# Kernel tuning notes

Hardware: AMD Instinct MI355X
Metric: run time of the kernel (lower is better)

The kernel has to match this reference:

```python
import jax, jax.numpy as jnp
import numpy as np

NUM_HEADS = 16
NUM_KV_HEADS = 2
HEAD_DIM = 256
HIDDEN = 2048
ROT_DIM = 64          # head_dim * partial_rotary_factor (0.25)
ROPE_THETA = 10000.0
EPS = 1e-6
T = 4096


def setup_inputs() -> dict:
    key = jax.random.key(0)
    k1, k2, k3, k4, k5 = jax.random.split(key, 5)
    qkv_out = HEAD_DIM * (NUM_HEADS * 2 + 2 * NUM_KV_HEADS)  # 9216 (q+gate, k, v)
    return {
        "hidden_states": jax.random.normal(k1, (T, HIDDEN), dtype=jnp.float32),
        "positions": jnp.arange(T, dtype=jnp.int32),
        "w_qkv": jax.random.normal(k2, (HIDDEN, qkv_out), dtype=jnp.float32) * 0.02,
        "w_o": jax.random.normal(k3, (NUM_HEADS * HEAD_DIM, HIDDEN), dtype=jnp.float32) * 0.02,
        "q_norm_w": jax.random.normal(k4, (HEAD_DIM,), dtype=jnp.float32) * 0.1,
        "k_norm_w": jax.random.normal(k5, (HEAD_DIM,), dtype=jnp.float32) * 0.1,
    }


def _gemma_rmsnorm(x, w):
    # GemmaRMSNorm: fp32 compute, scale by (1 + weight)
    xf = x.astype(jnp.float32)
    xf = xf * jax.lax.rsqrt(jnp.mean(xf * xf, axis=-1, keepdims=True) + EPS)
    return (xf * (1.0 + w.astype(jnp.float32))).astype(x.dtype)


def _apply_rope(x, positions):
    # neox-style partial RoPE on first ROT_DIM dims; x: [T, H, D]
    half = ROT_DIM // 2
    inv_freq = 1.0 / (ROPE_THETA ** (jnp.arange(0, ROT_DIM, 2, dtype=jnp.float32) / ROT_DIM))
    freqs = positions.astype(jnp.float32)[:, None] * inv_freq  # [T, half]
    cos = jnp.cos(freqs)[:, None, :]  # [T, 1, half]
    sin = jnp.sin(freqs)[:, None, :]
    x1 = x[..., :half]
    x2 = x[..., half:ROT_DIM]
    rot = jnp.concatenate([x1 * cos - x2 * sin, x2 * cos + x1 * sin], axis=-1)
    return jnp.concatenate([rot, x[..., ROT_DIM:]], axis=-1)


def reference(hidden_states, positions, w_qkv, w_o, q_norm_w, k_norm_w):
    q_size = NUM_HEADS * HEAD_DIM
    kv_size = NUM_KV_HEADS * HEAD_DIM
    qkv = hidden_states @ w_qkv  # [T, 2*q_size + 2*kv_size]

    # split q+gate (interleaved per head), k, v
    q_gate = qkv[:, : 2 * q_size].reshape(-1, NUM_HEADS, 2 * HEAD_DIM)
    q = q_gate[..., :HEAD_DIM]          # [T, H, D]
    gate = q_gate[..., HEAD_DIM:]       # [T, H, D]
    k = qkv[:, 2 * q_size : 2 * q_size + kv_size].reshape(-1, NUM_KV_HEADS, HEAD_DIM)
    v = qkv[:, 2 * q_size + kv_size :].reshape(-1, NUM_KV_HEADS, HEAD_DIM)

    # per-head QK RMSNorm then partial RoPE
    q = _apply_rope(_gemma_rmsnorm(q, q_norm_w), positions)
    k = _apply_rope(_gemma_rmsnorm(k, k_norm_w), positions)

    # GQA causal attention
    rep = NUM_HEADS // NUM_KV_HEADS
    k_rep = jnp.repeat(k, rep, axis=1)  # [T, H, D]
    v_rep = jnp.repeat(v, rep, axis=1)
    scaling = HEAD_DIM ** -0.5
    scores = jnp.einsum("qhd,khd->hqk", q, k_rep) * scaling  # [H, T, T]
    causal = positions[:, None] >= positions[None, :]
    scores = jnp.where(causal[None, :, :], scores, jnp.finfo(scores.dtype).min)
    probs = jax.nn.softmax(scores, axis=-1)
    attn = jnp.einsum("hqk,khd->qhd", probs, v_rep)  # [T, H, D]

    # sigmoid-gated output, then O projection
    attn = attn * jax.nn.sigmoid(gate)
    return attn.reshape(-1, NUM_HEADS * HEAD_DIM) @ w_o
```

## Files before the change

### kernel.cpp

```cpp
#include <hip/hip_runtime.h>

typedef __attribute__((ext_vector_type(4))) float f32x4;
typedef __attribute__((ext_vector_type(8))) __bf16 bf16x8;
typedef unsigned short ushort_t;
typedef unsigned int uint_t;
typedef __attribute__((ext_vector_type(4))) uint_t u32x4;

__device__ __forceinline__ float bf2f(ushort_t u) {
  union { uint_t i; float f; } v; v.i = ((uint_t)u) << 16; return v.f;
}
__device__ __forceinline__ ushort_t f2bf(float f) {
  union { float f; uint_t i; } v; v.f = f;
  uint_t x = v.i;
  return (ushort_t)((x + 0x7fffu + ((x >> 16) & 1u)) >> 16);
}

__device__ __forceinline__ void gload_lds16(const void* g, void* l) {
  __builtin_amdgcn_global_load_lds(
      (const __attribute__((address_space(1))) void*)g,
      (__attribute__((address_space(3))) void*)l, 16, 0, 0);
}

__global__ __launch_bounds__(256) void cast_bf16_kernel(
    const float* __restrict__ in, ushort_t* __restrict__ out, int n8) {
  int i = blockIdx.x * 256 + threadIdx.x;
  if (i >= n8) return;
  float4 a = ((const float4*)in)[i * 2];
  float4 b = ((const float4*)in)[i * 2 + 1];
  ushort4 o0 = make_ushort4(f2bf(a.x), f2bf(a.y), f2bf(a.z), f2bf(a.w));
  ushort4 o1 = make_ushort4(f2bf(b.x), f2bf(b.y), f2bf(b.z), f2bf(b.w));
  ((ushort4*)out)[i * 2] = o0;
  ((ushort4*)out)[i * 2 + 1] = o1;
}

__global__ __launch_bounds__(256) void transpose_cast_kernel(
    const float* __restrict__ in, ushort_t* __restrict__ out, int R, int C) {
  __shared__ float tile[32][33];
  int tx = threadIdx.x, ty = threadIdx.y;
  int c0 = blockIdx.x * 32, r0 = blockIdx.y * 32;
#pragma unroll
  for (int i = 0; i < 4; ++i)
    tile[ty + i * 8][tx] = in[(size_t)(r0 + ty + i * 8) * C + c0 + tx];
  __syncthreads();
#pragma unroll
  for (int i = 0; i < 4; ++i)
    out[(size_t)(c0 + ty + i * 8) * R + r0 + tx] = f2bf(tile[tx][ty + i * 8]);
}

template <int OUT_BF16>
__global__ __launch_bounds__(256, 2) void gemm_bt_kernel(
    const ushort_t* __restrict__ A, const ushort_t* __restrict__ BT,
    void* __restrict__ Cout, int M, int N, int K, int nx, int cpx) {
  const int lin = blockIdx.x;
  const int swz = (lin & 7) * cpx + (lin >> 3);
  const int bx = swz % nx, by = swz / nx;

  __shared__ ushort_t As[128 * 32];
  __shared__ ushort_t Bs[128 * 32];
  const int tid = threadIdx.x;
  const int lane = tid & 63;
  const int wid = tid >> 6;
  const int wr = wid >> 1, wc = wid & 1;
  const int qr = lane & 15, kg = lane >> 4;
  const size_t arow = (size_t)by * 128;
  const size_t brow = (size_t)bx * 128;

  f32x4 acc[4][4] = {};

  for (int k0 = 0; k0 < K; k0 += 32) {
    __syncthreads();
#pragma unroll
    for (int t = 0; t < 2; ++t) {
      int c = (t * 4 + wid) * 64 + lane;
      int r = c >> 2, kc = (c & 3) * 8;
      gload_lds16(A + (arow + r) * K + k0 + kc, &As[(t * 4 + wid) * 512]);
      gload_lds16(BT + (brow + r) * K + k0 + kc, &Bs[(t * 4 + wid) * 512]);
    }
    __syncthreads();
    bf16x8 af[4], bfr[4];
#pragma unroll
    for (int m = 0; m < 4; ++m)
      af[m] = *(const bf16x8*)&As[(wr * 64 + m * 16 + qr) * 32 + kg * 8];
#pragma unroll
    for (int n = 0; n < 4; ++n)
      bfr[n] = *(const bf16x8*)&Bs[(wc * 64 + n * 16 + qr) * 32 + kg * 8];
#pragma unroll
    for (int m = 0; m < 4; ++m)
#pragma unroll
      for (int n = 0; n < 4; ++n)
        acc[m][n] = __builtin_amdgcn_mfma_f32_16x16x32_bf16(af[m], bfr[n], acc[m][n], 0, 0, 0);
  }

#pragma unroll
  for (int m = 0; m < 4; ++m)
#pragma unroll
    for (int n = 0; n < 4; ++n)
#pragma unroll
      for (int j = 0; j < 4; ++j) {
        size_t row = arow + wr * 64 + m * 16 + kg * 4 + j;
        size_t col = brow + wc * 64 + n * 16 + qr;
        float v = acc[m][n][j];
        if (OUT_BF16) ((ushort_t*)Cout)[row * N + col] = f2bf(v);
        else ((float*)Cout)[row * N + col] = v;
      }
}

__global__ __launch_bounds__(256) void normrope_kernel(
    ushort_t* __restrict__ qkv, const int* __restrict__ positions,
    const float* __restrict__ qw, const float* __restrict__ kw) {
  const int wv = blockIdx.x * 4 + (threadIdx.x >> 6);
  const int lane = threadIdx.x & 63;
  const int t = wv / 18;
  const int idx = wv % 18;
  size_t base;
  const float* w;
  float sc;
  if (idx < 16) { base = (size_t)t * 9216 + idx * 512; w = qw; sc = 0.0625f; }
  else { base = (size_t)t * 9216 + 8192 + (size_t)(idx - 16) * 256; w = kw; sc = 1.0f; }

  ushort4 raw = *(const ushort4*)(qkv + base + lane * 4);
  float x0 = bf2f(raw.x), x1 = bf2f(raw.y), x2 = bf2f(raw.z), x3 = bf2f(raw.w);
  float ss = x0 * x0 + x1 * x1 + x2 * x2 + x3 * x3;
#pragma unroll
  for (int off = 1; off < 64; off <<= 1) ss += __shfl_xor(ss, off);
  float inv = rsqrtf(ss * (1.0f / 256.0f) + 1e-6f);
  const int d0 = lane * 4;
  float xn[4] = { x0 * inv * (1.f + w[d0]), x1 * inv * (1.f + w[d0 + 1]),
                  x2 * inv * (1.f + w[d0 + 2]), x3 * inv * (1.f + w[d0 + 3]) };
  float pn[4];
#pragma unroll
  for (int j = 0; j < 4; ++j) pn[j] = __shfl_xor(xn[j], 8);
  if (lane < 16) {
    const float pos = (float)positions[t];
#pragma unroll
    for (int j = 0; j < 4; ++j) {
      int d = d0 + j;
      int i = d & 31;
      float invf = __expf(-(float)i * 0.28782313662425574f);
      float fr = pos * invf;
      float s, c;
      sincosf(fr, &s, &c);
      xn[j] = (d < 32) ? (xn[j] * c - pn[j] * s) : (xn[j] * c + pn[j] * s);
    }
  }
  ushort4 o = make_ushort4(f2bf(xn[0] * sc), f2bf(xn[1] * sc),
                           f2bf(xn[2] * sc), f2bf(xn[3] * sc));
  *(ushort4*)(qkv + base + lane * 4) = o;
}

__global__ __launch_bounds__(256) void vtranspose_kernel(
    const ushort_t* __restrict__ qkv, ushort_t* __restrict__ VTg) {
  __shared__ ushort_t tile[32][34];
  const int tx = threadIdx.x, ty = threadIdx.y;
  const int t0 = blockIdx.x * 32, d0 = blockIdx.y * 32, kvh = blockIdx.z;
#pragma unroll
  for (int i = 0; i < 4; ++i) {
    int s = ty + i * 8;
    int kvl = ((s & 1) << 4) + ((s >> 3) << 2) + ((s & 7) >> 1);
    tile[s][tx] = qkv[(size_t)(t0 + kvl) * 9216 + 8704 + kvh * 256 + d0 + tx];
  }
  __syncthreads();
#pragma unroll
  for (int i = 0; i < 4; ++i)
    VTg[(size_t)kvh * 1048576 + (size_t)(d0 + ty + i * 8) * 4096 + t0 + tx] =
        tile[tx][ty + i * 8];
}

__device__ __forceinline__ bf16x8 softmax_group(
    f32x4 sA, f32x4 sB, int kv0, int qg, bool full,
    float& mr, float& lr, f32x4* o, int kg) {
  float v[8];
#pragma unroll
  for (int j = 0; j < 4; ++j) v[j] = sA[j];
#pragma unroll
  for (int j = 0; j < 4; ++j) v[4 + j] = sB[j];
  if (!full) {
#pragma unroll
    for (int j = 0; j < 4; ++j) {
      if (kv0 + kg * 4 + j > qg) v[j] = -1e30f;
      if (kv0 + 16 + kg * 4 + j > qg) v[4 + j] = -1e30f;
    }
  }
  float tm = v[0];
#pragma unroll
  for (int j = 1; j < 8; ++j) tm = fmaxf(tm, v[j]);
  tm = fmaxf(tm, __shfl_xor(tm, 16));
  tm = fmaxf(tm, __shfl_xor(tm, 32));
  float mref;
  if (__all(tm - mr <= 8.0f)) {
    mref = mr;
  } else {
    float mnew = fmaxf(mr, tm);
    float corr = __expf(mr - mnew);
    lr *= corr;
    float c0 = __shfl(corr, kg * 4 + 0);
    float c1 = __shfl(corr, kg * 4 + 1);
    float c2 = __shfl(corr, kg * 4 + 2);
    float c3 = __shfl(corr, kg * 4 + 3);
#pragma unroll
    for (int n = 0; n < 16; ++n) {
      o[n][0] *= c0; o[n][1] *= c1; o[n][2] *= c2; o[n][3] *= c3;
    }
    mr = mnew; mref = mnew;
  }
  float p[8];
#pragma unroll
  for (int j = 0; j < 8; ++j) p[j] = __expf(v[j] - mref);
  float ps = 0.f;
#pragma unroll
  for (int j = 0; j < 8; ++j) ps += p[j];
  ps += __shfl_xor(ps, 16);
  ps += __shfl_xor(ps, 32);
  lr += ps;
  union { u32x4 u; bf16x8 b; } pk;
#pragma unroll
  for (int u2 = 0; u2 < 4; ++u2)
    pk.u[u2] = (uint_t)f2bf(p[u2]) | ((uint_t)f2bf(p[4 + u2]) << 16);
  return pk.b;
}

__global__ __launch_bounds__(256, 2) void attn_kernel(
    const ushort_t* __restrict__ qkv, const ushort_t* __restrict__ VTg,
    ushort_t* __restrict__ A2) {
  const int id = blockIdx.x;
  const int g8 = id & 255, kk = id >> 8;
  const int x = g8 >> 4;
  const int h = ((g8 & 1) << 3) | ((g8 >> 1) & 7);
  const int qt = (3 - kk) * 16 + ((kk & 1) ? (15 - x) : x);
  const int kvh = g8 & 1;
  const int tid = threadIdx.x;
  const int lane = tid & 63;
  const int wid = tid >> 6;
  const int qr = lane & 15, kg = lane >> 4;

  __shared__ __align__(16) ushort_t Ks[2][32 * 256];
  __shared__ __align__(16) ushort_t Vt[2][256 * 32];

  const int q0 = qt * 64;
  const int myq0 = q0 + wid * 16;
  const ushort_t* vtg = VTg + (size_t)kvh * 1048576;

  bf16x8 qf[8];
#pragma unroll
  for (int kd = 0; kd < 8; ++kd)
    qf[kd] = *(const bf16x8*)(qkv + (size_t)(myq0 + qr) * 9216 + h * 512 +
                              kd * 32 + kg * 8);

  f32x4 o[16] = {};
  float mr = -1e30f, lr = 0.f;

  const int nt = qt * 2 + 2;

#pragma unroll
  for (int t = 0; t < 4; ++t) {
    int c = (t * 4 + wid) * 64 + lane;
    int r = c >> 5, dc = c & 31;
    int dcs = dc ^ (r & 7);
    gload_lds16(qkv + (size_t)r * 9216 + 8192 + kvh * 256 + dcs * 8,
                &Ks[0][(t * 4 + wid) * 512]);
  }
#pragma unroll
  for (int t = 0; t < 4; ++t) {
    int c = (t * 4 + wid) * 64 + lane;
    int d = c >> 2, k2 = c & 3;
    int kc = k2 ^ ((d >> 1) & 3);
    gload_lds16(vtg + (size_t)d * 4096 + kc * 8,
                &Vt[0][(t * 4 + wid) * 512]);
  }

  int buf = 0;
  for (int kt = 0; kt < nt; ++kt) {
    const int kv0 = kt * 32;
    __syncthreads();

    if (kt + 1 < nt) {
      const int kv0n = kv0 + 32;
#pragma unroll
      for (int t = 0; t < 4; ++t) {
        int c = (t * 4 + wid) * 64 + lane;
        int r = c >> 5, dc = c & 31;
        int dcs = dc ^ (r & 7);
        gload_lds16(qkv + (size_t)(kv0n + r) * 9216 + 8192 + kvh * 256 + dcs * 8,
                    &Ks[buf ^ 1][(t * 4 + wid) * 512]);
      }
#pragma unroll
      for (int t = 0; t < 4; ++t) {
        int c = (t * 4 + wid) * 64 + lane;
        int d = c >> 2, k2 = c & 3;
        int kc = k2 ^ ((d >> 1) & 3);
        gload_lds16(vtg + (size_t)d * 4096 + kv0n + kc * 8,
                    &Vt[buf ^ 1][(t * 4 + wid) * 512]);
      }
    }
    __builtin_amdgcn_sched_barrier(0);

    const bool active = (kv0 <= myq0 + 15);
    if (active) {
      const char* ksb = (const char*)&Ks[buf][0];
      const int kxor = (qr & 7) << 4;
      const int kbase = qr * 512;
      f32x4 s0 = {0.f, 0.f, 0.f, 0.f}, s1 = {0.f, 0.f, 0.f, 0.f};
      __builtin_amdgcn_s_setprio(1);
#pragma unroll
      for (int kd = 0; kd < 8; ++kd) {
        int off = kbase + ((kd * 64 + kg * 16) ^ kxor);
        bf16x8 kf0 = *(const bf16x8*)(ksb + off);
        bf16x8 kf1 = *(const bf16x8*)(ksb + off + 8192);
        s0 = __builtin_amdgcn_mfma_f32_16x16x32_bf16(kf0, qf[kd], s0, 0, 0, 0);
        s1 = __builtin_amdgcn_mfma_f32_16x16x32_bf16(kf1, qf[kd], s1, 0, 0, 0);
      }
      __builtin_amdgcn_s_setprio(0);

      const bool full = (kv0 + 31 <= myq0);
      bf16x8 pf = softmax_group(s0, s1, kv0, myq0 + qr, full, mr, lr, o, kg);

      const char* vtb = (const char*)&Vt[buf][0];
      const int vxor = (qr >> 1) & 3;
      __builtin_amdgcn_s_setprio(1);
#pragma unroll
      for (int n = 0; n < 16; ++n) {
        int dcol = n * 16 + qr;
        bf16x8 vf = *(const bf16x8*)(vtb + dcol * 64 + ((kg ^ vxor) * 16));
        o[n] = __builtin_amdgcn_mfma_f32_16x16x32_bf16(pf, vf, o[n], 0, 0, 0);
      }
      __builtin_amdgcn_s_setprio(0);
    }
    buf ^= 1;
  }

  float rl[4];
#pragma unroll
  for (int j = 0; j < 4; ++j) rl[j] = 1.0f / __shfl(lr, kg * 4 + j);
#pragma unroll
  for (int n = 0; n < 16; ++n) {
    int d = n * 16 + qr;
#pragma unroll
    for (int j = 0; j < 4; ++j) {
      int t = myq0 + kg * 4 + j;
      float val = o[n][j] * rl[j];
      float g2 = bf2f(qkv[(size_t)t * 9216 + h * 512 + 256 + d]);
      val *= 1.0f / (1.0f + __expf(-g2));
      A2[(size_t)t * 4096 + h * 256 + d] = f2bf(val);
    }
  }
}

extern "C" void kernel_launch(void* const* d_in, const int* in_sizes, int n_in,
                              void* d_out, int out_size, void* d_ws, size_t ws_size,
                              hipStream_t stream) {
  const float* hidden = (const float*)d_in[0];
  const int* positions = (const int*)d_in[1];
  const float* w_qkv = (const float*)d_in[2];
  const float* w_o = (const float*)d_in[3];
  const float* q_norm_w = (const float*)d_in[4];
  const float* k_norm_w = (const float*)d_in[5];

  char* ws = (char*)d_ws;
  ushort_t* hb    = (ushort_t*)ws;
  ushort_t* VTg   = (ushort_t*)ws;
  ushort_t* wqkvT = (ushort_t*)(ws + 16777216);
  ushort_t* woT   = (ushort_t*)(ws + 54525952);
  ushort_t* qkvb  = (ushort_t*)(ws + 71303168);
  ushort_t* A2    = (ushort_t*)(ws + 146800640);

  hipLaunchKernelGGL(cast_bf16_kernel, dim3(4096), dim3(256), 0, stream,
                     hidden, hb, 1048576);
  hipLaunchKernelGGL(transpose_cast_kernel, dim3(288, 64), dim3(32, 8), 0, stream,
                     w_qkv, wqkvT, 2048, 9216);
  hipLaunchKernelGGL(transpose_cast_kernel, dim3(64, 128), dim3(32, 8), 0, stream,
                     w_o, woT, 4096, 2048);
  hipLaunchKernelGGL((gemm_bt_kernel<1>), dim3(2304), dim3(256), 0, stream,
                     hb, wqkvT, (void*)qkvb, 4096, 9216, 2048, 72, 288);
  hipLaunchKernelGGL(normrope_kernel, dim3(18432), dim3(256), 0, stream,
                     qkvb, positions, q_norm_w, k_norm_w);
  hipLaunchKernelGGL(vtranspose_kernel, dim3(128, 8, 2), dim3(32, 8), 0, stream,
                     qkvb, VTg);
  hipLaunchKernelGGL(attn_kernel, dim3(1024), dim3(256), 0, stream,
                     qkvb, VTg, A2);
  hipLaunchKernelGGL((gemm_bt_kernel<0>), dim3(512), dim3(256), 0, stream,
                     A2, woT, d_out, 4096, 2048, 4096, 16, 64);
}
```

Before: 644.8 us.

## Add 256x256 eight-wave pipelined GEMM for QKV projection

Replaces the 128x128-tile GEMM for the QKV projection with a new 256x256-tile kernel using 8 waves per block. It uses 128KB LDS double buffering with swizzled layout, direct global-to-LDS loads interleaved with MFMA phases, and explicit barriers plus setprio scheduling. The aim is higher operand reuse and overlap of loads with compute. In exchange it carries large register and LDS pressure, and the K loop is hardcoded to 16 iterations, which matches K=2048 only.

```diff
diff --git a/kernel.cpp b/kernel.cpp
--- a/kernel.cpp
+++ b/kernel.cpp
@@ -102,6 +102,100 @@
         float v = acc[m][n][j];
         if (OUT_BF16) ((ushort_t*)Cout)[row * N + col] = f2bf(v);
         else ((float*)Cout)[row * N + col] = v;
+      }
+}
+
+#define G8_BAR() { __builtin_amdgcn_sched_barrier(0); __builtin_amdgcn_s_barrier(); __builtin_amdgcn_sched_barrier(0); }
+#define G8_RDA(base, mh) { _Pragma("unroll") for (int mm = 0; mm < 4; ++mm) { const int r_ = (base) + ((mh) * 64 + mm * 16 + qr) * 128; af[mm][0] = *(const bf16x8*)(smem + r_ + kgx0); af[mm][1] = *(const bf16x8*)(smem + r_ + kgx1); } }
+#define G8_RDB(base, nh) { _Pragma("unroll") for (int nn = 0; nn < 2; ++nn) { const int r_ = (base) + (rbo + (nh) * 32 + nn * 16 + qr) * 128; bfr[nn][0] = *(const bf16x8*)(smem + r_ + kgx0); bfr[nn][1] = *(const bf16x8*)(smem + r_ + kgx1); } }
+#define G8_MFMA(mh, nh) { __builtin_amdgcn_s_setprio(1); _Pragma("unroll") for (int mm = 0; mm < 4; ++mm) _Pragma("unroll") for (int nn = 0; nn < 2; ++nn) { f32x4 a_ = acc[(mh) * 4 + mm][(nh) * 2 + nn]; a_ = __builtin_amdgcn_mfma_f32_16x16x32_bf16(af[mm][0], bfr[nn][0], a_, 0, 0, 0); a_ = __builtin_amdgcn_mfma_f32_16x16x32_bf16(af[mm][1], bfr[nn][1], a_, 0, 0, 0); acc[(mh) * 4 + mm][(nh) * 2 + nn] = a_; } __builtin_amdgcn_s_setprio(0); }
+
+__global__ __launch_bounds__(512, 2) void gemm8_kernel(
+    const ushort_t* __restrict__ A, const ushort_t* __restrict__ BT,
+    ushort_t* __restrict__ C, int M, int N, int K, int nx, int cpx) {
+  __shared__ __align__(16) char smem[131072];
+  const int lin = blockIdx.x;
+  const int swz = (lin & 7) * cpx + (lin >> 3);
+  const int bx = swz % nx, by = swz / nx;
+  const int tid = threadIdx.x;
+  const int lane = tid & 63;
+  const int wid = tid >> 6;
+  const int wr = wid >> 2, wc = wid & 3;
+  const int qr = lane & 15, kg = lane >> 4;
+  const int rbo = (wc & 1) * 64;
+  const int kgx0 = (kg << 4) ^ ((qr & 7) << 4);
+  const int kgx1 = ((kg | 4) << 4) ^ ((qr & 7) << 4);
+  const int ab0 = wr * 16384, ab1 = 65536 + wr * 16384;
+  const int bb0 = 32768 + (wc >> 1) * 16384;
+  const int bb1 = 65536 + 32768 + (wc >> 1) * 16384;
+  const int srow = tid >> 3;
+  const int scol = ((tid & 7) ^ (srow & 7)) << 3;
+
+  const ushort_t* Ab = A + (size_t)(by * 256 + srow) * K + scol;
+  const ushort_t* Bb = BT + (size_t)(bx * 256 + srow) * K + scol;
+  const size_t r64 = (size_t)64 * K;
+  const size_t r128 = (size_t)128 * K;
+
+  f32x4 acc[8][4] = {};
+  bf16x8 af[4][2], bfr[2][2];
+
+  auto stA = [&](int h, int s, int rb) {
+    const ushort_t* p = Ab + (h ? r128 : 0) + s * 64;
+    gload_lds16(p, smem + rb + tid * 16);
+    gload_lds16(p + r64, smem + rb + 8192 + tid * 16);
+  };
+  auto stB = [&](int h, int s, int rb) {
+    const ushort_t* p = Bb + (h ? r128 : 0) + s * 64;
+    gload_lds16(p, smem + rb + tid * 16);
+    gload_lds16(p + r64, smem + rb + 8192 + tid * 16);
+  };
+
+  stA(0, 0, 0); stA(1, 0, 16384); stB(0, 0, 32768); stB(1, 0, 49152);
+  stA(0, 1, 65536); stA(1, 1, 81920);
+  asm volatile("s_waitcnt vmcnt(4)" ::: "memory");
+  G8_BAR()
+
+#pragma unroll 1
+  for (int it = 0; it < 16; ++it) {
+    const int e = it * 2;
+    const bool nl = (it < 15);
+    G8_RDA(ab0, 0) G8_RDB(bb0, 0)
+    stB(0, e + 1, 98304);
+    G8_BAR() G8_MFMA(0, 0) G8_BAR()
+    G8_RDB(bb0, 1)
+    stB(1, e + 1, 114688);
+    G8_BAR() G8_MFMA(0, 1) G8_BAR()
+    G8_RDA(ab0, 1)
+    G8_BAR() G8_MFMA(1, 1) G8_BAR()
+    G8_RDB(bb0, 0)
+    if (nl) { stA(0, e + 2, 0); stA(1, e + 2, 16384); }
+    G8_BAR() G8_MFMA(1, 0)
+    if (nl) { asm volatile("s_waitcnt vmcnt(4)" ::: "memory"); }
+    else    { asm volatile("s_waitcnt vmcnt(0)" ::: "memory"); }
+    G8_BAR()
+    G8_RDA(ab1, 0) G8_RDB(bb1, 0)
+    if (nl) { stB(0, e + 2, 32768); stB(1, e + 2, 49152); }
+    G8_BAR() G8_MFMA(0, 0) G8_BAR()
+    G8_RDB(bb1, 1)
+    G8_BAR() G8_MFMA(0, 1) G8_BAR()
+    G8_RDA(ab1, 1)
+    G8_BAR() G8_MFMA(1, 1) G8_BAR()
+    G8_RDB(bb1, 0)
+    if (nl) { stA(0, e + 3, 65536); stA(1, e + 3, 81920); }
+    G8_BAR() G8_MFMA(1, 0)
+    asm volatile("s_waitcnt vmcnt(4)" ::: "memory");
+    G8_BAR()
+  }
+
+#pragma unroll
+  for (int m = 0; m < 8; ++m)
+#pragma unroll
+    for (int n = 0; n < 4; ++n)
+#pragma unroll
+      for (int j = 0; j < 4; ++j) {
+        size_t row = (size_t)by * 256 + wr * 128 + m * 16 + kg * 4 + j;
+        size_t col = (size_t)bx * 256 + wc * 64 + n * 16 + qr;
+        C[row * N + col] = f2bf(acc[m][n][j]);
       }
 }
 
@@ -369,8 +463,8 @@
                      w_qkv, wqkvT, 2048, 9216);
   hipLaunchKernelGGL(transpose_cast_kernel, dim3(64, 128), dim3(32, 8), 0, stream,
                      w_o, woT, 4096, 2048);
-  hipLaunchKernelGGL((gemm_bt_kernel<1>), dim3(2304), dim3(256), 0, stream,
-                     hb, wqkvT, (void*)qkvb, 4096, 9216, 2048, 72, 288);
+  hipLaunchKernelGGL(gemm8_kernel, dim3(576), dim3(512), 0, stream,
+                     hb, wqkvT, qkvb, 4096, 9216, 2048, 36, 72);
   hipLaunchKernelGGL(normrope_kernel, dim3(18432), dim3(256), 0, stream,
                      qkvb, positions, q_norm_w, k_norm_w);
   hipLaunchKernelGGL(vtranspose_kernel, dim3(128, 8, 2), dim3(32, 8), 0, stream,
```

Measured after the change: 600.2 us. -6.9%, faster.
